# Optimization experiments

Measured on AMD Instinct MI355X. Metric: run time of the kernel, lower is better.

## Reference

```python
import jax, jax.numpy as jnp
import numpy as np

ROPE_BASE = 10000.0


def _rope(x):
    # x: (B, S, H, D) -- rotate-half RoPE applied per head over the sequence dim
    B, S, H, D = x.shape
    half = D // 2
    inv_freq = 1.0 / (ROPE_BASE ** (jnp.arange(half, dtype=jnp.float32) / half))
    ang = jnp.arange(S, dtype=jnp.float32)[:, None] * inv_freq[None, :]  # (S, half)
    cos = jnp.cos(ang)[None, :, None, :].astype(x.dtype)
    sin = jnp.sin(ang)[None, :, None, :].astype(x.dtype)
    x1, x2 = x[..., :half], x[..., half:]
    return jnp.concatenate([x1 * cos - x2 * sin, x2 * cos + x1 * sin], axis=-1)


def setup_inputs() -> dict:
    key = jax.random.key(0)
    ks = jax.random.split(key, 7)
    B, S, D = 8, 1024, 512
    HD = 512  # num_heads * key_dim = 8 * 64
    scale = 0.02
    return {
        "query": jax.random.normal(ks[0], (B, S, D), dtype=jnp.float32),
        "value": jax.random.normal(ks[1], (B, S, D), dtype=jnp.float32),
        "key_in": jax.random.normal(ks[2], (B, S, D), dtype=jnp.float32),
        "Wq": jax.random.normal(ks[3], (D, HD), dtype=jnp.float32) * scale,
        "Wk": jax.random.normal(ks[4], (D, HD), dtype=jnp.float32) * scale,
        "Wv": jax.random.normal(ks[5], (D, HD), dtype=jnp.float32) * scale,
        "Wo": jax.random.normal(ks[6], (HD, D), dtype=jnp.float32) * scale,
    }


def reference(query, value, key_in, Wq, Wk, Wv, Wo):
    H, Dh = 8, 64
    B, Sq, _ = query.shape
    Sk = key_in.shape[1]
    # QKV projections, split heads: (B, S, H, Dh)
    q = (query @ Wq).reshape(B, Sq, H, Dh)
    v = (value @ Wv).reshape(B, Sk, H, Dh)
    k = (key_in @ Wk).reshape(B, Sk, H, Dh)
    # inline RoPE on q and k (applied before head transpose, as in the original)
    q = _rope(q)
    k = _rope(k)
    # scaled dot-product attention with causal mask
    q = q * (1.0 / jnp.sqrt(jnp.asarray(Dh, q.dtype)))
    scores = jnp.einsum("bqhd,bkhd->bhqk", q, k)  # (B, H, Sq, Sk)
    causal = jnp.tril(jnp.ones((Sq, Sk), dtype=bool))[None, None]
    scores = jnp.where(causal, scores, jnp.asarray(-1e9, scores.dtype))
    probs = jax.nn.softmax(scores, axis=-1)
    out = jnp.einsum("bhqk,bkhd->bqhd", probs, v)  # (B, Sq, H, Dh)
    out = out.reshape(B, Sq, H * Dh) @ Wo  # output projection
    return out
```

## Files before the change

### kernel.cpp

```cpp
#include <hip/hip_runtime.h>
#include <hip/hip_bf16.h>
#include <stdint.h>

#define DEV static __device__ __forceinline__

typedef __attribute__((ext_vector_type(8)))  short    s16x8;
typedef __attribute__((ext_vector_type(4)))  short    s16x4;
typedef __attribute__((ext_vector_type(8)))  __bf16   bf16x8;
typedef __attribute__((ext_vector_type(2)))  __bf16   bf16x2;
typedef __attribute__((ext_vector_type(4)))  float    f32x4;
typedef __attribute__((ext_vector_type(16))) float    f32x16;
typedef __attribute__((ext_vector_type(2)))  unsigned u32x2;
typedef __attribute__((ext_vector_type(4)))  unsigned u32x4;

#define WAIT_VMCNT(N) do{ asm volatile("s_waitcnt vmcnt(" #N ")" ::: "memory"); \
                          __builtin_amdgcn_sched_barrier(0); }while(0)
DEV void barrier_raw(){ __builtin_amdgcn_sched_barrier(0); __builtin_amdgcn_s_barrier(); }

DEV short f2b(float f){
  union{float f; uint32_t i;} x; x.f = f;
  uint32_t r = x.i + 0x7FFFu + ((x.i >> 16) & 1u);
  return (short)(r >> 16);
}
DEV unsigned packbf(float a, float b){
  bf16x2 v = { (__bf16)a, (__bf16)b };
  return __builtin_bit_cast(unsigned, v);
}
DEV bf16x8 as_bf(s16x8 v){ return __builtin_bit_cast(bf16x8, v); }
DEV float fexp2(float x){ return __builtin_amdgcn_exp2f(x); }
DEV f32x4 mf(s16x8 a, s16x8 b, f32x4 c){
  return __builtin_amdgcn_mfma_f32_16x16x32_bf16(as_bf(a), as_bf(b), c, 0, 0, 0);
}
DEV f32x16 mf32(s16x8 a, s16x8 b, f32x16 c){
  return __builtin_amdgcn_mfma_f32_32x32x16_bf16(as_bf(a), as_bf(b), c, 0, 0, 0);
}

DEV void gload_lds16(const void* g, void* l){
  __builtin_amdgcn_global_load_lds((const __attribute__((address_space(1))) void*)g,
                                   (__attribute__((address_space(3))) void*)l, 16, 0, 0);
}

#if __has_builtin(__builtin_amdgcn_permlane32_swap)
DEV void pswap2(unsigned a, unsigned b, unsigned& x, unsigned& y){
  u32x2 rr = __builtin_amdgcn_permlane32_swap(a, b, false, false);
  x = rr[0]; y = rr[1];
}
DEV float partner32(float v, int hi){
  unsigned u = __builtin_bit_cast(unsigned, v);
  u32x2 rr = __builtin_amdgcn_permlane32_swap(u, u, false, false);
  return __builtin_bit_cast(float, hi ? rr[0] : rr[1]);
}
#else
DEV void pswap2(unsigned a, unsigned b, unsigned& x, unsigned& y){
  unsigned pa_ = (unsigned)__shfl_xor((int)a, 32, 64);
  unsigned pb_ = (unsigned)__shfl_xor((int)b, 32, 64);
  int lo = ((threadIdx.x & 63) < 32);
  x = lo ? a   : pb_;
  y = lo ? pa_ : b;
}
DEV float partner32(float v, int hi){ (void)hi; return __shfl_xor(v, 32, 64); }
#endif

__global__ __launch_bounds__(256) void k_conv3(const float* __restrict__ q,
                                               const float* __restrict__ k,
                                               const float* __restrict__ v,
                                               short* __restrict__ out){
  int z = blockIdx.z;
  const float* in = (z == 0) ? q : (z == 1) ? k : v;
  int i = (blockIdx.x * 256 + threadIdx.x) * 4;
  float4 val = *(const float4*)(in + i);
  short o[4] = { f2b(val.x), f2b(val.y), f2b(val.z), f2b(val.w) };
  *(uint2*)(out + (size_t)z * 4194304 + i) = *(uint2*)o;
}

__global__ __launch_bounds__(256) void k_wt4(const float* __restrict__ w0,
                                             const float* __restrict__ w1,
                                             const float* __restrict__ w2,
                                             const float* __restrict__ w3,
                                             short* __restrict__ wt){
  __shared__ float tile[32][33];
  int z = blockIdx.z;
  const float* w = (z == 0) ? w0 : (z == 1) ? w1 : (z == 2) ? w2 : w3;
  short* o = wt + (size_t)z * 262144;
  int bx = blockIdx.x * 32, by = blockIdx.y * 32;
  int tx = threadIdx.x, ty = threadIdx.y;
  for (int j = 0; j < 32; j += 8)
    tile[ty + j][tx] = w[(size_t)(by + ty + j) * 512 + bx + tx];
  __syncthreads();
  for (int j = 0; j < 32; j += 8)
    o[(size_t)(bx + ty + j) * 512 + by + tx] = f2b(tile[tx][ty + j]);
}

__global__ __launch_bounds__(256) void k_table(float* __restrict__ tab){
  int idx = blockIdx.x * 256 + threadIdx.x;
  int s = idx >> 5, j = idx & 31;
  float inv = __expf(-(float)j * (1.0f / 32.0f) * logf(10000.0f));
  float ang = (float)s * inv;
  tab[idx * 2 + 0] = cosf(ang);
  tab[idx * 2 + 1] = sinf(ang);
}

__global__ __launch_bounds__(256) void k_qkv(const short* __restrict__ Xb,
                                             const short* __restrict__ Wcat,
                                             const float* __restrict__ tab,
                                             short* __restrict__ Qa,
                                             short* __restrict__ Ka,
                                             short* __restrict__ Vt){
  __shared__ __align__(16) short Al[3][4096];
  __shared__ __align__(16) short Bl[3][4096];
  const int t = threadIdx.x, w = t >> 6, lane = t & 63, fr = lane & 15, fg = lane >> 4;
  const int sel = blockIdx.y >> 2;
  const short* X = Xb + (size_t)sel * 4194304;
  const int bm = blockIdx.x * 128, bn = blockIdx.y * 128;
  const int wm = (w >> 1) * 64, wn = (w & 1) * 64;

  auto stage = [&](int buf, int k0){
#pragma unroll
    for (int q = 0; q < 2; q++){
      int lin = q * 256 + t;
      int row = lin >> 2, sl = lin & 3;
      int gs = (sl ^ (row & 3)) * 8;
      gload_lds16(X    + (size_t)(bm + row) * 512 + k0 + gs, &Al[buf][(q * 256 + w * 64) * 8]);
      gload_lds16(Wcat + (size_t)(bn + row) * 512 + k0 + gs, &Bl[buf][(q * 256 + w * 64) * 8]);
    }
  };

  f32x4 acc[4][4] = {};
  stage(0, 0);
  stage(1, 32);
  for (int t16 = 0; t16 < 16; ++t16){
    barrier_raw();
    int kc = t16 + 2; if (kc > 15) kc = 15;
    stage((t16 + 2) % 3, kc * 32);
    WAIT_VMCNT(8);
    barrier_raw();
    const int cur = t16 % 3;
    s16x8 af[4], bv[4];
#pragma unroll
    for (int f = 0; f < 4; f++){
      int ra = wm + f * 16 + fr;
      af[f] = *(const s16x8*)(&Al[cur][ra * 32 + ((fg ^ (ra & 3)) * 8)]);
      int rb = wn + f * 16 + fr;
      bv[f] = *(const s16x8*)(&Bl[cur][rb * 32 + ((fg ^ (rb & 3)) * 8)]);
    }
#pragma unroll
    for (int i = 0; i < 4; i++)
#pragma unroll
      for (int jj = 0; jj < 4; jj++)
        acc[i][jj] = mf(af[i], bv[jj], acc[i][jj]);
  }

  const int row0 = bm + wm + fg * 4;
  const int b = row0 >> 10;
  const int s_base = row0 & 1023;
  const int hh = (((blockIdx.y & 3) * 128) + wn) >> 6;
  if (sel < 2){
    const float scale = (sel == 0) ? 0.125f * 1.44269504f : 1.0f;
    short* out = (sel == 0) ? Qa : Ka;
#pragma unroll
    for (int i = 0; i < 4; i++)
#pragma unroll
      for (int jj = 0; jj < 2; jj++){
        int d = jj * 16 + fr;
#pragma unroll
        for (int r = 0; r < 4; r++){
          int s = s_base + i * 16 + r;
          float2 cs = *(const float2*)(tab + (size_t)(s * 32 + d) * 2);
          float x1 = acc[i][jj][r], x2 = acc[i][jj + 2][r];
          size_t ob = ((size_t)((b * 8 + hh) * 1024 + s)) * 64 + d;
          out[ob]      = f2b((x1 * cs.x - x2 * cs.y) * scale);
          out[ob + 32] = f2b((x2 * cs.x + x1 * cs.y) * scale);
        }
      }
  } else {
#pragma unroll
    for (int i = 0; i < 4; i++)
#pragma unroll
      for (int jj = 0; jj < 4; jj++){
        int d = jj * 16 + fr;
        s16x4 pk;
#pragma unroll
        for (int r = 0; r < 4; r++) pk[r] = f2b(acc[i][jj][r]);
        size_t ob = ((size_t)((b * 8 + hh) * 64 + d)) * 1024 + s_base + i * 16;
        *(s16x4*)(Vt + ob) = pk;
      }
  }
}

__global__ __launch_bounds__(256) void k_attn(const short* __restrict__ Qb,
                                              const short* __restrict__ Kb,
                                              const short* __restrict__ Vt,
                                              short* __restrict__ O){
  __shared__ __align__(16) short KL[3][4096];
  __shared__ __align__(16) short VL[3][4096];
  const int bid = blockIdx.x;
  const int BiMap[8] = {7,6,5,4, 0,1,2,3};
  const int Bi = BiMap[bid >> 6];
  const int bh = bid & 63;
  const int B0 = Bi * 128;
  const int nch = (B0 >> 6) + 2;
  const int t = threadIdx.x, w = t >> 6, lane = t & 63;
  const int col = lane & 31, hi = lane >> 5;
  const short* Qp = Qb + (size_t)bh * 65536;
  const short* Kp = Kb + (size_t)bh * 65536;
  const short* Vp = Vt + (size_t)bh * 65536;
  const int qrow = B0 + 4 * col + w;

  s16x8 qb[4];
#pragma unroll
  for (int ks = 0; ks < 4; ks++)
    qb[ks] = *(const s16x8*)(Qp + (size_t)qrow * 64 + ks * 16 + hi * 8);

  int crow[16];
#pragma unroll
  for (int r = 0; r < 16; r++) crow[r] = (r & 3) + 8 * (r >> 2) + 4 * hi;

  f32x16 oacc[2] = {};
  float m = -1e30f, l = 0.f;

  auto stage = [&](int buf, int kv0){
#pragma unroll
    for (int R = 0; R < 2; R++){
      int lin = R * 256 + w * 64 + lane;
      int row = lin >> 3, slot = lin & 7;
      int gs = ((slot ^ (row & 7)) * 8);
      gload_lds16(Kp + (size_t)(kv0 + row) * 64 + gs, &KL[buf][(R * 256 + w * 64) * 8]);
      gload_lds16(Vp + (size_t)row * 1024 + kv0 + gs, &VL[buf][(R * 256 + w * 64) * 8]);
    }
  };

  stage(0, 0);
  stage(1, (nch > 1 ? 64 : 0));

  for (int i = 0; i < nch; ++i){
    const int kv0 = i * 64;
    barrier_raw();
    int kc = i + 2; if (kc > nch - 1) kc = nch - 1;
    stage((i + 2) % 3, kc * 64);
    WAIT_VMCNT(8);
    barrier_raw();
    const int cur = i % 3;
    __builtin_amdgcn_s_setprio(1);
    f32x16 sc[2];
#pragma unroll
    for (int f = 0; f < 2; f++){
      f32x16 s = {};
      int row = f * 32 + col, rx = row & 7;
#pragma unroll
      for (int ks = 0; ks < 4; ks++){
        s16x8 ka = *(const s16x8*)(&KL[cur][row * 64 + ((ks * 2 + hi) ^ rx) * 8]);
        s = mf32(ka, qb[ks], s);
      }
      sc[f] = s;
    }
    __builtin_amdgcn_s_setprio(0);
    if (kv0 >= B0){
#pragma unroll
      for (int f = 0; f < 2; f++)
#pragma unroll
        for (int r = 0; r < 16; r++){
          int kv = kv0 + f * 32 + crow[r];
          if (kv > qrow) sc[f][r] = -1e30f;
        }
    }
    float mx[16];
#pragma unroll
    for (int r = 0; r < 16; r++) mx[r] = fmaxf(sc[0][r], sc[1][r]);
#pragma unroll
    for (int off = 8; off >= 1; off >>= 1)
#pragma unroll
      for (int r = 0; r < off; r++) mx[r] = fmaxf(mx[r], mx[r + off]);
    float tm = fmaxf(mx[0], partner32(mx[0], hi));
    if (!__all(tm <= m + 8.f)){
      float mn = fmaxf(m, tm);
      float corr = fexp2(m - mn);
      m = mn;
      l *= corr;
      float cpv[16];
#pragma unroll
      for (int r = 0; r < 16; r++) cpv[r] = __shfl(corr, crow[r], 64);
#pragma unroll
      for (int r = 0; r < 16; r++){ oacc[0][r] *= cpv[r]; oacc[1][r] *= cpv[r]; }
    }
    float p[32];
#pragma unroll
    for (int f = 0; f < 2; f++)
#pragma unroll
      for (int i2 = 0; i2 < 16; i2++) p[f * 16 + i2] = fexp2(sc[f][i2] - m);
    unsigned wq[2][8];
#pragma unroll
    for (int f = 0; f < 2; f++)
#pragma unroll
      for (int i2 = 0; i2 < 8; i2++)
        wq[f][i2] = packbf(p[f * 16 + 2 * i2], p[f * 16 + 2 * i2 + 1]);
#pragma unroll
    for (int off = 16; off >= 1; off >>= 1)
#pragma unroll
      for (int r = 0; r < off; r++) p[r] += p[r + off];
    l += p[0] + partner32(p[0], hi);
    s16x8 pa[4];
#pragma unroll
    for (int f = 0; f < 2; f++)
#pragma unroll
      for (int half = 0; half < 2; half++){
        unsigned w0, w1, w2, w3;
        pswap2(wq[f][half * 4 + 0], wq[f][half * 4 + 2], w0, w2);
        pswap2(wq[f][half * 4 + 1], wq[f][half * 4 + 3], w1, w3);
        u32x4 uv = { w0, w1, w2, w3 };
        pa[f * 2 + half] = __builtin_bit_cast(s16x8, uv);
      }
    __builtin_amdgcn_s_setprio(1);
#pragma unroll
    for (int ks = 0; ks < 4; ks++)
#pragma unroll
      for (int df = 0; df < 2; df++){
        int row = df * 32 + col;
        s16x8 vb = *(const s16x8*)(&VL[cur][row * 64 + ((ks * 2 + hi) ^ (row & 7)) * 8]);
        oacc[df] = mf32(pa[ks], vb, oacc[df]);
      }
    __builtin_amdgcn_s_setprio(0);
  }

  const int b = bh >> 3, h = bh & 7;
  float lf[16];
#pragma unroll
  for (int r = 0; r < 16; r++) lf[r] = __shfl(l, crow[r], 64);
#pragma unroll
  for (int r = 0; r < 16; r++){
    int qq = B0 + 4 * crow[r] + w;
    float inv = 1.0f / lf[r];
    O[(size_t)(b * 1024 + qq) * 512 + h * 64 + col]      = f2b(oacc[0][r] * inv);
    O[(size_t)(b * 1024 + qq) * 512 + h * 64 + 32 + col] = f2b(oacc[1][r] * inv);
  }
}

__global__ __launch_bounds__(256) void k_gemm_out(const short* __restrict__ X,
                                                  const short* __restrict__ Wt,
                                                  float* __restrict__ C){
  __shared__ __align__(16) short Al[3][8192];
  __shared__ __align__(16) short Bl[3][8192];
  const int t = threadIdx.x;
  const int w = t >> 6, lane = t & 63, fr = lane & 15, fg = lane >> 4;
  const int bm = blockIdx.x * 128, bn = blockIdx.y * 128;
  const int wm = (w >> 1) * 64, wn = (w & 1) * 64;

  auto stage = [&](int buf, int k0){
#pragma unroll
    for (int q = 0; q < 4; q++){
      int lin = q * 256 + t;
      int row = lin >> 3, sl = lin & 7;
      int gs = (sl ^ (row & 7)) * 8;
      gload_lds16(X  + (size_t)(bm + row) * 512 + k0 + gs, &Al[buf][(q * 256 + w * 64) * 8]);
      gload_lds16(Wt + (size_t)(bn + row) * 512 + k0 + gs, &Bl[buf][(q * 256 + w * 64) * 8]);
    }
  };

  f32x4 acc[4][4] = {};
  stage(0, 0);
  stage(1, 64);
  for (int t8 = 0; t8 < 8; ++t8){
    barrier_raw();
    int kc = t8 + 2; if (kc > 7) kc = 7;
    stage((t8 + 2) % 3, kc * 64);
    WAIT_VMCNT(16);
    barrier_raw();
    const int cur = t8 % 3;
#pragma unroll
    for (int kk = 0; kk < 2; kk++){
      s16x8 af[4], bv[4];
#pragma unroll
      for (int f = 0; f < 4; f++){
        int rowa = wm + f * 16 + fr;
        af[f] = *(const s16x8*)(&Al[cur][rowa * 64 + ((kk * 4 + fg) ^ (rowa & 7)) * 8]);
        int rowb = wn + f * 16 + fr;
        bv[f] = *(const s16x8*)(&Bl[cur][rowb * 64 + ((kk * 4 + fg) ^ (rowb & 7)) * 8]);
      }
#pragma unroll
      for (int i = 0; i < 4; i++)
#pragma unroll
        for (int jj = 0; jj < 4; jj++)
          acc[i][jj] = mf(af[i], bv[jj], acc[i][jj]);
    }
  }
  const int row0 = bm + wm + fg * 4;
  const int col0 = bn + wn + fr;
#pragma unroll
  for (int i = 0; i < 4; i++)
#pragma unroll
    for (int jj = 0; jj < 4; jj++)
#pragma unroll
      for (int r = 0; r < 4; r++)
        C[(size_t)(row0 + i * 16 + r) * 512 + col0 + jj * 16] = acc[i][jj][r];
}

extern "C" void kernel_launch(void* const* d_in, const int* in_sizes, int n_in,
                              void* d_out, int out_size, void* d_ws, size_t ws_size,
                              hipStream_t stream){
  const float* query  = (const float*)d_in[0];
  const float* value  = (const float*)d_in[1];
  const float* key_in = (const float*)d_in[2];
  const float* Wq     = (const float*)d_in[3];
  const float* Wk     = (const float*)d_in[4];
  const float* Wv     = (const float*)d_in[5];
  const float* Wo     = (const float*)d_in[6];

  char* ws = (char*)d_ws;
  const size_t MB = 1ull << 20;
  short* Xb   = (short*)(ws);
  short* Wcat = (short*)(ws + 24 * MB);
  float* tab  = (float*)(ws + 26 * MB);
  short* Qa   = (short*)(ws + 26 * MB + 256 * 1024);
  short* Ka   = (short*)((char*)Qa + 8 * MB);
  short* Va   = (short*)((char*)Ka + 8 * MB);
  short* Oa   = Xb;
  short* Wot  = Wcat + 786432;

  k_conv3<<<dim3(4096, 1, 3), 256, 0, stream>>>(query, key_in, value, Xb);
  k_wt4<<<dim3(16, 16, 4), dim3(32, 8), 0, stream>>>(Wq, Wk, Wv, Wo, Wcat);
  k_table<<<128, 256, 0, stream>>>(tab);

  k_qkv<<<dim3(64, 12), 256, 0, stream>>>(Xb, Wcat, tab, Qa, Ka, Va);

  k_attn<<<512, 256, 0, stream>>>(Qa, Ka, Va, Oa);

  k_gemm_out<<<dim3(64, 4), 256, 0, stream>>>(Oa, Wot, (float*)d_out);
}
```

Measured before the change: 80.99 us.

## Split attention KV range across two wave groups and drop LDS staging

```diff
diff --git a/kernel.cpp b/kernel.cpp
--- a/kernel.cpp
+++ b/kernel.cpp
@@ -129,11 +129,10 @@
   stage(0, 0);
   stage(1, 32);
   for (int t16 = 0; t16 < 16; ++t16){
+    WAIT_VMCNT(4);
     barrier_raw();
     int kc = t16 + 2; if (kc > 15) kc = 15;
     stage((t16 + 2) % 3, kc * 32);
-    WAIT_VMCNT(8);
-    barrier_raw();
     const int cur = t16 % 3;
     s16x8 af[4], bv[4];
 #pragma unroll
@@ -187,24 +186,25 @@
   }
 }
 
-__global__ __launch_bounds__(256) void k_attn(const short* __restrict__ Qb,
-                                              const short* __restrict__ Kb,
-                                              const short* __restrict__ Vt,
-                                              short* __restrict__ O){
-  __shared__ __align__(16) short KL[3][4096];
-  __shared__ __align__(16) short VL[3][4096];
+__global__ __launch_bounds__(512, 4) void k_attn(const short* __restrict__ Qb,
+                                                 const short* __restrict__ Kb,
+                                                 const short* __restrict__ Vt,
+                                                 short* __restrict__ O){
+  __shared__ float O1L[128][64];
+  __shared__ float mL[128], lL[128];
   const int bid = blockIdx.x;
-  const int BiMap[8] = {7,6,5,4, 0,1,2,3};
-  const int Bi = BiMap[bid >> 6];
   const int bh = bid & 63;
-  const int B0 = Bi * 128;
-  const int nch = (B0 >> 6) + 2;
+  const int k8 = bid >> 6;
+  const int ti = (k8 < 4) ? (7 - k8) : (k8 - 4);
+  const int T0 = ti * 128;
+  const int nchg = ti + 1;
   const int t = threadIdx.x, w = t >> 6, lane = t & 63;
+  const int g = w >> 2, wsub = w & 3;
   const int col = lane & 31, hi = lane >> 5;
   const short* Qp = Qb + (size_t)bh * 65536;
   const short* Kp = Kb + (size_t)bh * 65536;
   const short* Vp = Vt + (size_t)bh * 65536;
-  const int qrow = B0 + 4 * col + w;
+  const int qrow = T0 + 4 * col + wsub;
 
   s16x8 qb[4];
 #pragma unroll
@@ -218,43 +218,23 @@
   f32x16 oacc[2] = {};
   float m = -1e30f, l = 0.f;
 
-  auto stage = [&](int buf, int kv0){
-#pragma unroll
-    for (int R = 0; R < 2; R++){
-      int lin = R * 256 + w * 64 + lane;
-      int row = lin >> 3, slot = lin & 7;
-      int gs = ((slot ^ (row & 7)) * 8);
-      gload_lds16(Kp + (size_t)(kv0 + row) * 64 + gs, &KL[buf][(R * 256 + w * 64) * 8]);
-      gload_lds16(Vp + (size_t)row * 1024 + kv0 + gs, &VL[buf][(R * 256 + w * 64) * 8]);
-    }
-  };
-
-  stage(0, 0);
-  stage(1, (nch > 1 ? 64 : 0));
-
-  for (int i = 0; i < nch; ++i){
-    const int kv0 = i * 64;
-    barrier_raw();
-    int kc = i + 2; if (kc > nch - 1) kc = nch - 1;
-    stage((i + 2) % 3, kc * 64);
-    WAIT_VMCNT(8);
-    barrier_raw();
-    const int cur = i % 3;
+  for (int c = 0; c < nchg; ++c){
+    const int kv0 = (2 * c + g) * 64;
     __builtin_amdgcn_s_setprio(1);
     f32x16 sc[2];
 #pragma unroll
     for (int f = 0; f < 2; f++){
+      int row = f * 32 + col;
       f32x16 s = {};
-      int row = f * 32 + col, rx = row & 7;
 #pragma unroll
       for (int ks = 0; ks < 4; ks++){
-        s16x8 ka = *(const s16x8*)(&KL[cur][row * 64 + ((ks * 2 + hi) ^ rx) * 8]);
+        s16x8 ka = *(const s16x8*)(Kp + (size_t)(kv0 + row) * 64 + (ks * 2 + hi) * 8);
         s = mf32(ka, qb[ks], s);
       }
       sc[f] = s;
     }
     __builtin_amdgcn_s_setprio(0);
-    if (kv0 >= B0){
+    if (kv0 >= T0){
 #pragma unroll
       for (int f = 0; f < 2; f++)
 #pragma unroll
@@ -263,11 +243,12 @@
           if (kv > qrow) sc[f][r] = -1e30f;
         }
     }
-    float mx[16];
-#pragma unroll
-    for (int r = 0; r < 16; r++) mx[r] = fmaxf(sc[0][r], sc[1][r]);
-#pragma unroll
-    for (int off = 8; off >= 1; off >>= 1)
+    float mx[8];
+#pragma unroll
+    for (int r = 0; r < 8; r++)
+      mx[r] = fmaxf(fmaxf(sc[0][r], sc[0][r + 8]), fmaxf(sc[1][r], sc[1][r + 8]));
+#pragma unroll
+    for (int off = 4; off >= 1; off >>= 1)
 #pragma unroll
       for (int r = 0; r < off; r++) mx[r] = fmaxf(mx[r], mx[r + off]);
     float tm = fmaxf(mx[0], partner32(mx[0], hi));
@@ -282,22 +263,27 @@
 #pragma unroll
       for (int r = 0; r < 16; r++){ oacc[0][r] *= cpv[r]; oacc[1][r] *= cpv[r]; }
     }
-    float p[32];
 #pragma unroll
     for (int f = 0; f < 2; f++)
 #pragma unroll
-      for (int i2 = 0; i2 < 16; i2++) p[f * 16 + i2] = fexp2(sc[f][i2] - m);
+      for (int i2 = 0; i2 < 16; i2++) sc[f][i2] = fexp2(sc[f][i2] - m);
     unsigned wq[2][8];
 #pragma unroll
     for (int f = 0; f < 2; f++)
 #pragma unroll
       for (int i2 = 0; i2 < 8; i2++)
-        wq[f][i2] = packbf(p[f * 16 + 2 * i2], p[f * 16 + 2 * i2 + 1]);
-#pragma unroll
-    for (int off = 16; off >= 1; off >>= 1)
-#pragma unroll
-      for (int r = 0; r < off; r++) p[r] += p[r + off];
-    l += p[0] + partner32(p[0], hi);
+        wq[f][i2] = packbf(sc[f][2 * i2], sc[f][2 * i2 + 1]);
+    {
+      f32x16 sv = sc[0] + sc[1];
+      float s8[8];
+#pragma unroll
+      for (int r = 0; r < 8; r++) s8[r] = sv[r] + sv[r + 8];
+#pragma unroll
+      for (int off = 4; off >= 1; off >>= 1)
+#pragma unroll
+        for (int r = 0; r < off; r++) s8[r] += s8[r + off];
+      l += s8[0] + partner32(s8[0], hi);
+    }
     s16x8 pa[4];
 #pragma unroll
     for (int f = 0; f < 2; f++)
@@ -314,23 +300,41 @@
     for (int ks = 0; ks < 4; ks++)
 #pragma unroll
       for (int df = 0; df < 2; df++){
-        int row = df * 32 + col;
-        s16x8 vb = *(const s16x8*)(&VL[cur][row * 64 + ((ks * 2 + hi) ^ (row & 7)) * 8]);
+        s16x8 vb = *(const s16x8*)(Vp + (size_t)(df * 32 + col) * 1024 + kv0 + (ks * 2 + hi) * 8);
         oacc[df] = mf32(pa[ks], vb, oacc[df]);
       }
     __builtin_amdgcn_s_setprio(0);
   }
 
-  const int b = bh >> 3, h = bh & 7;
-  float lf[16];
-#pragma unroll
-  for (int r = 0; r < 16; r++) lf[r] = __shfl(l, crow[r], 64);
-#pragma unroll
-  for (int r = 0; r < 16; r++){
-    int qq = B0 + 4 * crow[r] + w;
-    float inv = 1.0f / lf[r];
-    O[(size_t)(b * 1024 + qq) * 512 + h * 64 + col]      = f2b(oacc[0][r] * inv);
-    O[(size_t)(b * 1024 + qq) * 512 + h * 64 + 32 + col] = f2b(oacc[1][r] * inv);
+  if (g == 1){
+#pragma unroll
+    for (int r = 0; r < 16; r++){
+      int rr = crow[r];
+      O1L[4 * rr + wsub][col]      = oacc[0][r];
+      O1L[4 * rr + wsub][32 + col] = oacc[1][r];
+    }
+    if (hi == 0){ mL[4 * col + wsub] = m; lL[4 * col + wsub] = l; }
+  }
+  __syncthreads();
+  if (g == 0){
+    float m1 = mL[4 * col + wsub], l1 = lL[4 * col + wsub];
+    float ms = fmaxf(m, m1);
+    float c0 = fexp2(m - ms), c1 = fexp2(m1 - ms);
+    float ln = c0 * l + c1 * l1;
+    const int b = bh >> 3, h = bh & 7;
+#pragma unroll
+    for (int r = 0; r < 16; r++){
+      int rr = crow[r];
+      float c0f = __shfl(c0, rr, 64);
+      float c1f = __shfl(c1, rr, 64);
+      float lnf = __shfl(ln, rr, 64);
+      float inv = 1.0f / lnf;
+      int qq = T0 + 4 * rr + wsub;
+      float o0 = (c0f * oacc[0][r] + c1f * O1L[4 * rr + wsub][col])      * inv;
+      float o1 = (c0f * oacc[1][r] + c1f * O1L[4 * rr + wsub][32 + col]) * inv;
+      O[(size_t)(b * 1024 + qq) * 512 + h * 64 + col]      = f2b(o0);
+      O[(size_t)(b * 1024 + qq) * 512 + h * 64 + 32 + col] = f2b(o1);
+    }
   }
 }
 
@@ -359,11 +363,10 @@
   stage(0, 0);
   stage(1, 64);
   for (int t8 = 0; t8 < 8; ++t8){
+    WAIT_VMCNT(8);
     barrier_raw();
     int kc = t8 + 2; if (kc > 7) kc = 7;
     stage((t8 + 2) % 3, kc * 64);
-    WAIT_VMCNT(16);
-    barrier_raw();
     const int cur = t8 % 3;
 #pragma unroll
     for (int kk = 0; kk < 2; kk++){
@@ -421,7 +424,7 @@
 
   k_qkv<<<dim3(64, 12), 256, 0, stream>>>(Xb, Wcat, tab, Qa, Ka, Va);
 
-  k_attn<<<512, 256, 0, stream>>>(Qa, Ka, Va, Oa);
+  k_attn<<<512, 512, 0, stream>>>(Qa, Ka, Va, Oa);
 
   k_gemm_out<<<dim3(64, 4), 256, 0, stream>>>(Oa, Wot, (float*)d_out);
 }
```

Result: slower. 96.40 us (+19.0%).
